# Performance work log

Measured on AMD Instinct MI355X. Metric: run time of the kernel, lower is better.

Reference implementation:

```python
import jax, jax.numpy as jnp
import numpy as np

DIM = 256
N_EMBED = 16384


def setup_inputs() -> dict:
    key = jax.random.key(0)
    k1, k2 = jax.random.split(key)
    z = jax.random.normal(k1, (16, DIM, 32, 32), dtype=jnp.float32)
    # nn.Embedding weight init: uniform(-1/n_embed, 1/n_embed)
    codebook = jax.random.uniform(
        k2, (N_EMBED, DIM), dtype=jnp.float32,
        minval=-1.0 / N_EMBED, maxval=1.0 / N_EMBED)
    return {"z": z, "codebook": codebook}


def reference(z, codebook):
    # b c h w -> b h w c
    zp = jnp.transpose(z, (0, 2, 3, 1))  # [B,H,W,C]
    b, h, w, c = zp.shape
    zf = zp.reshape(-1, c)  # [N, dim]
    # ||z||^2 + ||e||^2 - 2 z.e  -> [N, n_embed]
    d = (jnp.sum(zf * zf, axis=1, keepdims=True)
         + jnp.sum(codebook * codebook, axis=1)
         - 2.0 * jnp.einsum('nd,kd->nk', zf, codebook))
    idx = jnp.argmin(d, axis=1)  # [N]
    z_q = codebook[idx].reshape(b, h, w, c)
    return z_q, idx
```

## Files before the change

kernel.cpp:

```cpp
#include <hip/hip_runtime.h>


#define NQ 16384
#define NE 16384
#define DIM 256

typedef __attribute__((ext_vector_type(8))) _Float16 half8;
typedef __attribute__((ext_vector_type(4))) float floatx4;

__device__ __forceinline__ float fm(float a, float b) { return __fmul_rn(a, b); }
__device__ __forceinline__ float fa(float a, float b) { return __fadd_rn(a, b); }
__device__ __forceinline__ float fs(float a, float b) { return __fsub_rn(a, b); }

#define GLOAD_LDS16(gp, lp)                                                  \
    __builtin_amdgcn_global_load_lds(                                        \
        (const __attribute__((address_space(1))) void*)(gp),                 \
        (__attribute__((address_space(3))) void*)(lp), 16, 0, 0)

__global__ __launch_bounds__(256) void prep_z(const float* __restrict__ z,
                                              _Float16* __restrict__ zh,
                                              float* __restrict__ zn) {
    const int bid = blockIdx.x;
    const int t = threadIdx.x;
    if (bid < 4096) {
        __shared__ float tile[32][33];
        const int b  = bid >> 8;
        const int c0 = ((bid >> 5) & 7) * 32;
        const int n0 = (bid & 31) * 32;
        const int tx = t & 31, ty = t >> 5;
        const float* zb = z + (size_t)b * 256 * 1024;
        #pragma unroll
        for (int j = 0; j < 32; j += 8)
            tile[ty + j][tx] = zb[(size_t)(c0 + ty + j) * 1024 + n0 + tx];
        __syncthreads();
        #pragma unroll
        for (int j = 0; j < 32; j += 8)
            zh[(size_t)(b * 1024 + n0 + ty + j) * 256 + c0 + tx] =
                (_Float16)tile[tx][ty + j];
    } else {
        const int row = (bid - 4096) * 256 + t;
        const float* p = z + ((size_t)(row >> 10) * 256) * 1024 + (row & 1023);
        float half_[2];
        #pragma unroll
        for (int h = 0; h < 2; ++h) {
            const int c0 = h * 128;
            float r[8], v;
            #pragma unroll
            for (int j = 0; j < 8; j++) { v = p[(size_t)(c0 + j) << 10]; r[j] = fm(v, v); }
            #pragma unroll
            for (int i = 8; i < 128; i += 8)
                #pragma unroll
                for (int j = 0; j < 8; j++) {
                    v = p[(size_t)(c0 + i + j) << 10];
                    r[j] = fa(r[j], fm(v, v));
                }
            half_[h] = fa(fa(fa(r[0], r[1]), fa(r[2], r[3])),
                          fa(fa(r[4], r[5]), fa(r[6], r[7])));
        }
        zn[row] = fa(half_[0], half_[1]);
    }
}

__global__ __launch_bounds__(256) void prep_e(const float* __restrict__ cb,
                                              _Float16* __restrict__ eh,
                                              float* __restrict__ en) {
    const int bid = blockIdx.x;
    const int t = threadIdx.x;
    if (bid < 4096) {
        const size_t i = ((size_t)bid * 256 + t) * 4;
        const float4 v = *(const float4*)(cb + i);
        _Float16 o[4] = { (_Float16)(v.x * 16384.0f), (_Float16)(v.y * 16384.0f),
                          (_Float16)(v.z * 16384.0f), (_Float16)(v.w * 16384.0f) };
        *(ushort4*)(eh + i) = *(const ushort4*)o;
    } else {
        const int row = (bid - 4096) * 256 + t;
        const float* p = cb + (size_t)row * DIM;
        float half_[2];
        #pragma unroll
        for (int h = 0; h < 2; ++h) {
            const float* q = p + h * 128;
            float r[8];
            #pragma unroll
            for (int j = 0; j < 8; j++) r[j] = fm(q[j], q[j]);
            #pragma unroll
            for (int i = 8; i < 128; i += 8)
                #pragma unroll
                for (int j = 0; j < 8; j++) r[j] = fa(r[j], fm(q[i + j], q[i + j]));
            half_[h] = fa(fa(fa(r[0], r[1]), fa(r[2], r[3])),
                          fa(fa(r[4], r[5]), fa(r[6], r[7])));
        }
        en[row] = fa(half_[0], half_[1]);
    }
}

__device__ __forceinline__ void merge3(unsigned& a0, unsigned& a1, unsigned& a2,
                                       unsigned b0, unsigned b1, unsigned b2) {
    const unsigned m0 = min(a0, b0);
    const unsigned x  = max(a0, b0);
    const unsigned p  = min(a1, b1);
    const unsigned q  = max(a1, b1);
    const unsigned m1 = min(x, p);
    const unsigned m2 = min(max(x, p), min(q, min(a2, b2)));
    a0 = m0; a1 = m1; a2 = m2;
}

__global__ __launch_bounds__(256, 2) void gemm_top3(
    const _Float16* __restrict__ zh, const _Float16* __restrict__ eh,
    const float* __restrict__ en, unsigned* __restrict__ part)
{
    __shared__ __align__(16) _Float16 lds[2][16384];
    unsigned* mbuf = (unsigned*)&lds[0][0];

    const int t = threadIdx.x;
    const int lane = t & 63, w = t >> 6;
    const int wr = w >> 1, wc = w & 1;
    const int q4 = lane >> 4, c4 = lane & 15;
    const int m0 = blockIdx.x * 128;
    const int g0 = blockIdx.y * 512;

    unsigned trip[16][3];
    #pragma unroll
    for (int s = 0; s < 16; ++s)
        trip[s][0] = trip[s][1] = trip[s][2] = 0xFFFFFFFFu;

    int sm[4], sg[4];
    #pragma unroll
    for (int p = 0; p < 4; ++p) {
        const int s = p * 256 + t;
        sm[p] = s >> 3;
        sg[p] = (s & 7) ^ (sm[p] & 7);
    }
    const int ldsb = w * 64 * 8;

    {
        const int n0 = g0, kb = 0;
        #pragma unroll
        for (int p = 0; p < 4; ++p) {
            GLOAD_LDS16(zh + (size_t)(m0 + sm[p]) * 256 + kb + sg[p] * 8,
                        &lds[0][(p * 256) * 8 + ldsb]);
            GLOAD_LDS16(eh + (size_t)(n0 + sm[p]) * 256 + kb + sg[p] * 8,
                        &lds[0][8192 + (p * 256) * 8 + ldsb]);
        }
    }

    floatx4 acc[4][4];
    for (int it = 0; it < 16; ++it) {
        const int sub = it >> 2;
        const int buf = it & 1;
        const int n0 = g0 + sub * 128;

        if ((it & 3) == 0) {
            #pragma unroll
            for (int i = 0; i < 4; i++)
                #pragma unroll
                for (int j = 0; j < 4; j++) acc[i][j] = (floatx4){0.f, 0.f, 0.f, 0.f};
        }

        __syncthreads();

        if (it + 1 < 16) {
            const int subn = (it + 1) >> 2;
            const int kbn  = ((it + 1) & 3) * 64;
            const int n0n  = g0 + subn * 128;
            _Float16* dst = &lds[buf ^ 1][0];
            #pragma unroll
            for (int p = 0; p < 4; ++p) {
                GLOAD_LDS16(zh + (size_t)(m0 + sm[p]) * 256 + kbn + sg[p] * 8,
                            dst + (p * 256) * 8 + ldsb);
                GLOAD_LDS16(eh + (size_t)(n0n + sm[p]) * 256 + kbn + sg[p] * 8,
                            dst + 8192 + (p * 256) * 8 + ldsb);
            }
        }

        const _Float16* Ab = &lds[buf][0];
        const _Float16* Bb = &lds[buf][8192];
        #pragma unroll
        for (int kk = 0; kk < 2; ++kk) {
            half8 a[4], b[4];
            #pragma unroll
            for (int i = 0; i < 4; ++i) {
                const int m  = wr * 64 + i * 16 + c4;
                const int gs = (kk * 4 + q4) ^ (m & 7);
                a[i] = *(const half8*)&Ab[(size_t)(m * 8 + gs) * 8];
            }
            #pragma unroll
            for (int j = 0; j < 4; ++j) {
                const int n  = wc * 64 + j * 16 + c4;
                const int gs = (kk * 4 + q4) ^ (n & 7);
                b[j] = *(const half8*)&Bb[(size_t)(n * 8 + gs) * 8];
            }
            #pragma unroll
            for (int i = 0; i < 4; ++i)
                #pragma unroll
                for (int j = 0; j < 4; ++j)
                    acc[i][j] = __builtin_amdgcn_mfma_f32_16x16x32_f16(
                        a[i], b[j], acc[i][j], 0, 0, 0);
        }

        if ((it & 3) == 3) {
            float en2[4]; unsigned cp[4];
            #pragma unroll
            for (int j = 0; j < 4; ++j) {
                const int col = n0 + wc * 64 + j * 16 + c4;
                en2[j] = en[col] * 1048576.0f;
                cp[j]  = (131072u << 14) + (unsigned)col;
            }
            #pragma unroll
            for (int i = 0; i < 4; ++i)
                #pragma unroll
                for (int r = 0; r < 4; ++r) {
                    const int v0 = (int)__builtin_fmaf(acc[i][0][r], -128.0f, en2[0]);
                    const int v1 = (int)__builtin_fmaf(acc[i][1][r], -128.0f, en2[1]);
                    const int v2 = (int)__builtin_fmaf(acc[i][2][r], -128.0f, en2[2]);
                    const int v3 = (int)__builtin_fmaf(acc[i][3][r], -128.0f, en2[3]);
                    const unsigned k0 = ((unsigned)v0 << 14) + cp[0];
                    const unsigned k1 = ((unsigned)v1 << 14) + cp[1];
                    const unsigned k2 = ((unsigned)v2 << 14) + cp[2];
                    const unsigned k3 = ((unsigned)v3 << 14) + cp[3];
                    const unsigned l01 = min(k0, k1), h01 = max(k0, k1);
                    const unsigned l23 = min(k2, k3), h23 = max(k2, k3);
                    const unsigned s0  = min(l01, l23);
                    const unsigned m1  = max(l01, l23), m2 = min(h01, h23);
                    const unsigned s1  = min(m1, m2),  s2 = max(m1, m2);
                    merge3(trip[i * 4 + r][0], trip[i * 4 + r][1], trip[i * 4 + r][2],
                           s0, s1, s2);
                }
        }
    }

    #pragma unroll
    for (int s = 0; s < 16; ++s) {
        unsigned t0 = trip[s][0], t1 = trip[s][1], t2 = trip[s][2];
        #pragma unroll
        for (int msk = 1; msk < 16; msk <<= 1) {
            const unsigned u0 = (unsigned)__shfl_xor((int)t0, msk, 64);
            const unsigned u1 = (unsigned)__shfl_xor((int)t1, msk, 64);
            const unsigned u2 = (unsigned)__shfl_xor((int)t2, msk, 64);
            merge3(t0, t1, t2, u0, u1, u2);
        }
        if (c4 < 3) {
            const int row = wr * 64 + (s >> 2) * 16 + q4 * 4 + (s & 3);
            mbuf[(row * 2 + wc) * 3 + c4] = (c4 == 0) ? t0 : ((c4 == 1) ? t1 : t2);
        }
    }
    __syncthreads();
    if (t < 128) {
        unsigned a0 = mbuf[(t * 2 + 0) * 3 + 0];
        unsigned a1 = mbuf[(t * 2 + 0) * 3 + 1];
        unsigned a2 = mbuf[(t * 2 + 0) * 3 + 2];
        merge3(a0, a1, a2, mbuf[(t * 2 + 1) * 3 + 0],
               mbuf[(t * 2 + 1) * 3 + 1], mbuf[(t * 2 + 1) * 3 + 2]);
        unsigned* pp = part + (size_t)(m0 + t) * 96 + blockIdx.y * 3;
        pp[0] = a0; pp[1] = a1; pp[2] = a2;
    }
}

__global__ __launch_bounds__(256) void resolve(
    const unsigned* __restrict__ part, const float* __restrict__ z,
    const float* __restrict__ cb, const float* __restrict__ zn,
    const float* __restrict__ en, float* __restrict__ out_zq,
    float* __restrict__ out_idx)
{
    const int w = threadIdx.x >> 6, lane = threadIdx.x & 63;
    const int row = blockIdx.x * 4 + w;
    __shared__ unsigned candbuf[4][16];

    const unsigned* pr = part + (size_t)row * 96;
    const unsigned k1 = pr[lane];
    const unsigned k2 = (lane < 32) ? pr[64 + lane] : 0xFFFFFFFFu;
    unsigned vm = min(k1, k2);
    #pragma unroll
    for (int m = 1; m < 64; m <<= 1)
        vm = min(vm, (unsigned)__shfl_xor((int)vm, m, 64));
    const unsigned vlim = (vm >> 14) + 84u;
    const bool s1 = (k1 >> 14) <= vlim;
    const bool s2 = (lane < 32) && ((k2 >> 14) <= vlim);
    const unsigned long long b1 = __ballot(s1);
    const unsigned long long b2 = __ballot(s2);
    const unsigned long long below = (1ull << lane) - 1ull;
    const int pos1 = __popcll(b1 & below);
    const int pos2 = __popcll(b1) + __popcll(b2 & below);
    int ncand = __popcll(b1) + __popcll(b2);
    if (ncand > 16) ncand = 16;

    if (lane < 16) candbuf[w][lane] = 0;
    __syncthreads();
    if (s1 && pos1 < 16) candbuf[w][pos1] = k1 & 16383u;
    if (s2 && pos2 < 16) candbuf[w][pos2] = k2 & 16383u;
    __syncthreads();

    const int ci = lane >> 2, l = lane & 3;
    const bool act = ci < ncand;
    const unsigned idxc = candbuf[w][ci];
    const float* zb  = z + ((size_t)(row >> 10) * 256) * 1024 + (row & 1023);
    const float* cbr = cb + (size_t)idxc * 256;
    float s = 0.f;
    #pragma unroll
    for (int ch = 0; ch < 16; ++ch)
        #pragma unroll
        for (int v = 3; v >= 0; --v) {
            const int cd = ch * 16 + v * 4 + l;
            s = fa(fm(zb[(size_t)cd << 10], cbr[cd]), s);
        }
    const int base = lane & ~3;
    const float s0 = __shfl(s, base + 0, 64);
    const float sA = __shfl(s, base + 1, 64);
    const float sB = __shfl(s, base + 2, 64);
    const float sC = __shfl(s, base + 3, 64);
    const float cross = fa(fa(s0, sA), fa(sB, sC));
    const float d = fs(fa(zn[row], en[idxc]), fm(2.0f, cross));
    unsigned long long key = act
        ? (((unsigned long long)__float_as_uint(d) << 32) | idxc) : ~0ull;
    #pragma unroll
    for (int m = 1; m < 64; m <<= 1) {
        const unsigned long long o =
            (unsigned long long)__shfl_xor((long long)key, m, 64);
        if (o < key) key = o;
    }
    const int widx = (int)(key & 0xFFFFFFFFu);
    *(float4*)(out_zq + (size_t)row * 256 + lane * 4) =
        *(const float4*)(cb + (size_t)widx * 256 + lane * 4);
    if (lane == 0) out_idx[row] = (float)widx;
}

extern "C" void kernel_launch(void* const* d_in, const int* in_sizes, int n_in,
                              void* d_out, int out_size, void* d_ws, size_t ws_size,
                              hipStream_t stream) {
    const float* z  = (const float*)d_in[0];
    const float* cb = (const float*)d_in[1];
    float* out = (float*)d_out;

    char* ws = (char*)d_ws;
    _Float16* zh = (_Float16*)ws;
    _Float16* eh = (_Float16*)(ws + (size_t)8388608);
    float* zn  = (float*)(ws + (size_t)16777216);
    float* en  = (float*)(ws + (size_t)16842752);
    unsigned* part = (unsigned*)(ws + (size_t)16908288);

    prep_z<<<4160, 256, 0, stream>>>(z, zh, zn);
    prep_e<<<4160, 256, 0, stream>>>(cb, eh, en);
    gemm_top3<<<dim3(128, 32), 256, 0, stream>>>(zh, eh, en, part);
    resolve<<<4096, 256, 0, stream>>>(part, z, cb, zn, en, out,
                                      out + (size_t)NQ * DIM);
}
```

Before: 375.1 us.

## Merge prep kernels, halve GEMM K-tile for 3 blocks/CU, stage z row in LDS

```diff
diff --git a/kernel.cpp b/kernel.cpp
--- a/kernel.cpp
+++ b/kernel.cpp
@@ -17,9 +17,12 @@
         (const __attribute__((address_space(1))) void*)(gp),                 \
         (__attribute__((address_space(3))) void*)(lp), 16, 0, 0)
 
-__global__ __launch_bounds__(256) void prep_z(const float* __restrict__ z,
-                                              _Float16* __restrict__ zh,
-                                              float* __restrict__ zn) {
+__global__ __launch_bounds__(256) void prep(const float* __restrict__ z,
+                                            const float* __restrict__ cb,
+                                            _Float16* __restrict__ zh,
+                                            _Float16* __restrict__ eh,
+                                            float* __restrict__ zn,
+                                            float* __restrict__ en) {
     const int bid = blockIdx.x;
     const int t = threadIdx.x;
     if (bid < 4096) {
@@ -37,7 +40,7 @@
         for (int j = 0; j < 32; j += 8)
             zh[(size_t)(b * 1024 + n0 + ty + j) * 256 + c0 + tx] =
                 (_Float16)tile[tx][ty + j];
-    } else {
+    } else if (bid < 4160) {
         const int row = (bid - 4096) * 256 + t;
         const float* p = z + ((size_t)(row >> 10) * 256) * 1024 + (row & 1023);
         float half_[2];
@@ -58,22 +61,14 @@
                           fa(fa(r[4], r[5]), fa(r[6], r[7])));
         }
         zn[row] = fa(half_[0], half_[1]);
-    }
-}
-
-__global__ __launch_bounds__(256) void prep_e(const float* __restrict__ cb,
-                                              _Float16* __restrict__ eh,
-                                              float* __restrict__ en) {
-    const int bid = blockIdx.x;
-    const int t = threadIdx.x;
-    if (bid < 4096) {
-        const size_t i = ((size_t)bid * 256 + t) * 4;
+    } else if (bid < 8256) {
+        const size_t i = ((size_t)(bid - 4160) * 256 + t) * 4;
         const float4 v = *(const float4*)(cb + i);
         _Float16 o[4] = { (_Float16)(v.x * 16384.0f), (_Float16)(v.y * 16384.0f),
                           (_Float16)(v.z * 16384.0f), (_Float16)(v.w * 16384.0f) };
         *(ushort4*)(eh + i) = *(const ushort4*)o;
     } else {
-        const int row = (bid - 4096) * 256 + t;
+        const int row = (bid - 8256) * 256 + t;
         const float* p = cb + (size_t)row * DIM;
         float half_[2];
         #pragma unroll
@@ -104,11 +99,11 @@
     a0 = m0; a1 = m1; a2 = m2;
 }
 
-__global__ __launch_bounds__(256, 2) void gemm_top3(
+__global__ __launch_bounds__(256, 3) void gemm_top3(
     const _Float16* __restrict__ zh, const _Float16* __restrict__ eh,
     const float* __restrict__ en, unsigned* __restrict__ part)
 {
-    __shared__ __align__(16) _Float16 lds[2][16384];
+    __shared__ __align__(16) _Float16 lds[2][8192];
     unsigned* mbuf = (unsigned*)&lds[0][0];
 
     const int t = threadIdx.x;
@@ -123,33 +118,32 @@
     for (int s = 0; s < 16; ++s)
         trip[s][0] = trip[s][1] = trip[s][2] = 0xFFFFFFFFu;
 
-    int sm[4], sg[4];
-    #pragma unroll
-    for (int p = 0; p < 4; ++p) {
+    int sm[2], sg[2];
+    #pragma unroll
+    for (int p = 0; p < 2; ++p) {
         const int s = p * 256 + t;
-        sm[p] = s >> 3;
-        sg[p] = (s & 7) ^ (sm[p] & 7);
+        sm[p] = s >> 2;
+        sg[p] = ((s & 3) - (sm[p] >> 1)) & 3;
     }
     const int ldsb = w * 64 * 8;
 
     {
-        const int n0 = g0, kb = 0;
-        #pragma unroll
-        for (int p = 0; p < 4; ++p) {
-            GLOAD_LDS16(zh + (size_t)(m0 + sm[p]) * 256 + kb + sg[p] * 8,
+        #pragma unroll
+        for (int p = 0; p < 2; ++p) {
+            GLOAD_LDS16(zh + (size_t)(m0 + sm[p]) * 256 + sg[p] * 8,
                         &lds[0][(p * 256) * 8 + ldsb]);
-            GLOAD_LDS16(eh + (size_t)(n0 + sm[p]) * 256 + kb + sg[p] * 8,
-                        &lds[0][8192 + (p * 256) * 8 + ldsb]);
+            GLOAD_LDS16(eh + (size_t)(g0 + sm[p]) * 256 + sg[p] * 8,
+                        &lds[0][4096 + (p * 256) * 8 + ldsb]);
         }
     }
 
     floatx4 acc[4][4];
-    for (int it = 0; it < 16; ++it) {
-        const int sub = it >> 2;
+    for (int it = 0; it < 32; ++it) {
+        const int sub = it >> 3;
         const int buf = it & 1;
         const int n0 = g0 + sub * 128;
 
-        if ((it & 3) == 0) {
+        if ((it & 7) == 0) {
             #pragma unroll
             for (int i = 0; i < 4; i++)
                 #pragma unroll
@@ -158,36 +152,35 @@
 
         __syncthreads();
 
-        if (it + 1 < 16) {
-            const int subn = (it + 1) >> 2;
-            const int kbn  = ((it + 1) & 3) * 64;
+        if (it + 1 < 32) {
+            const int subn = (it + 1) >> 3;
+            const int kbn  = ((it + 1) & 7) * 32;
             const int n0n  = g0 + subn * 128;
             _Float16* dst = &lds[buf ^ 1][0];
             #pragma unroll
-            for (int p = 0; p < 4; ++p) {
+            for (int p = 0; p < 2; ++p) {
                 GLOAD_LDS16(zh + (size_t)(m0 + sm[p]) * 256 + kbn + sg[p] * 8,
                             dst + (p * 256) * 8 + ldsb);
                 GLOAD_LDS16(eh + (size_t)(n0n + sm[p]) * 256 + kbn + sg[p] * 8,
-                            dst + 8192 + (p * 256) * 8 + ldsb);
+                            dst + 4096 + (p * 256) * 8 + ldsb);
             }
         }
 
         const _Float16* Ab = &lds[buf][0];
-        const _Float16* Bb = &lds[buf][8192];
-        #pragma unroll
-        for (int kk = 0; kk < 2; ++kk) {
+        const _Float16* Bb = &lds[buf][4096];
+        {
             half8 a[4], b[4];
             #pragma unroll
             for (int i = 0; i < 4; ++i) {
                 const int m  = wr * 64 + i * 16 + c4;
-                const int gs = (kk * 4 + q4) ^ (m & 7);
-                a[i] = *(const half8*)&Ab[(size_t)(m * 8 + gs) * 8];
+                const int sa = m * 4 + ((q4 + (m >> 1)) & 3);
+                a[i] = *(const half8*)&Ab[sa * 8];
             }
             #pragma unroll
             for (int j = 0; j < 4; ++j) {
                 const int n  = wc * 64 + j * 16 + c4;
-                const int gs = (kk * 4 + q4) ^ (n & 7);
-                b[j] = *(const half8*)&Bb[(size_t)(n * 8 + gs) * 8];
+                const int sb = n * 4 + ((q4 + (n >> 1)) & 3);
+                b[j] = *(const half8*)&Bb[sb * 8];
             }
             #pragma unroll
             for (int i = 0; i < 4; ++i)
@@ -197,7 +190,7 @@
                         a[i], b[j], acc[i][j], 0, 0, 0);
         }
 
-        if ((it & 3) == 3) {
+        if ((it & 7) == 7) {
             float en2[4]; unsigned cp[4];
             #pragma unroll
             for (int j = 0; j < 4; ++j) {
@@ -263,7 +256,13 @@
 {
     const int w = threadIdx.x >> 6, lane = threadIdx.x & 63;
     const int row = blockIdx.x * 4 + w;
+    __shared__ float zrow[4][256];
     __shared__ unsigned candbuf[4][16];
+
+    const float* zb = z + ((size_t)(row >> 10) * 256) * 1024 + (row & 1023);
+    #pragma unroll
+    for (int k = 0; k < 4; ++k)
+        zrow[w][lane + 64 * k] = zb[(size_t)(lane + 64 * k) << 10];
 
     const unsigned* pr = part + (size_t)row * 96;
     const unsigned k1 = pr[lane];
@@ -292,7 +291,6 @@
     const int ci = lane >> 2, l = lane & 3;
     const bool act = ci < ncand;
     const unsigned idxc = candbuf[w][ci];
-    const float* zb  = z + ((size_t)(row >> 10) * 256) * 1024 + (row & 1023);
     const float* cbr = cb + (size_t)idxc * 256;
     float s = 0.f;
     #pragma unroll
@@ -300,7 +298,7 @@
         #pragma unroll
         for (int v = 3; v >= 0; --v) {
             const int cd = ch * 16 + v * 4 + l;
-            s = fa(fm(zb[(size_t)cd << 10], cbr[cd]), s);
+            s = fa(fm(zrow[w][cd], cbr[cd]), s);
         }
     const int base = lane & ~3;
     const float s0 = __shfl(s, base + 0, 64);
@@ -337,8 +335,7 @@
     float* en  = (float*)(ws + (size_t)16842752);
     unsigned* part = (unsigned*)(ws + (size_t)16908288);
 
-    prep_z<<<4160, 256, 0, stream>>>(z, zh, zn);
-    prep_e<<<4160, 256, 0, stream>>>(cb, eh, en);
+    prep<<<8320, 256, 0, stream>>>(z, cb, zh, eh, zn, en);
     gemm_top3<<<dim3(128, 32), 256, 0, stream>>>(zh, eh, en, part);
     resolve<<<4096, 256, 0, stream>>>(part, z, cb, zn, en, out,
                                       out + (size_t)NQ * DIM);
```

Result: faster. 337.3 us (-10.1%).
